# Optimization experiments

Measured on AMD Instinct MI355X. Metric: run time of the kernel, lower is better.

Reference implementation:

```python
import jax, jax.numpy as jnp
import numpy as np

N = 100000
E = 1600000
IN_DIM = 128
HID = 128
OUT = 8


def _linear_params(key, fan_in, fan_out, bias=True):
    k1, k2 = jax.random.split(key)
    bound = 1.0 / np.sqrt(fan_in)
    W = jax.random.uniform(k1, (fan_in, fan_out), jnp.float32, -bound, bound)
    if bias:
        b = jax.random.uniform(k2, (fan_out,), jnp.float32, -bound, bound)
        return W, b
    return W


def setup_inputs() -> dict:
    key = jax.random.key(0)
    ks = jax.random.split(key, 20)
    x = jax.random.normal(ks[0], (N, IN_DIM), jnp.float32)
    edge_index = jax.random.randint(ks[1], (2, E), 0, N, jnp.int64)
    y = jax.random.randint(ks[2], (N,), 0, 2, jnp.int64)
    pmp_mask = jax.random.randint(ks[3], (N,), 0, 2, jnp.int64).astype(jnp.bool_)
    # layer 1 params
    W_fr1 = _linear_params(ks[4], IN_DIM, HID, bias=False)
    W_be1 = _linear_params(ks[5], IN_DIM, HID, bias=False)
    alpha_w1, alpha_b1 = _linear_params(ks[6], IN_DIM, 1)
    Wself_w1, Wself_b1 = _linear_params(ks[7], IN_DIM, HID)
    # layer 2 params
    W_fr2 = _linear_params(ks[8], HID, HID, bias=False)
    W_be2 = _linear_params(ks[9], HID, HID, bias=False)
    alpha_w2, alpha_b2 = _linear_params(ks[10], HID, 1)
    Wself_w2, Wself_b2 = _linear_params(ks[11], HID, HID)
    # classifier
    cls_w, cls_b = _linear_params(ks[12], HID, OUT)
    return dict(x=x, edge_index=edge_index, y=y, pmp_mask=pmp_mask,
                W_fr1=W_fr1, W_be1=W_be1, alpha_w1=alpha_w1, alpha_b1=alpha_b1,
                Wself_w1=Wself_w1, Wself_b1=Wself_b1,
                W_fr2=W_fr2, W_be2=W_be2, alpha_w2=alpha_w2, alpha_b2=alpha_b2,
                Wself_w2=Wself_w2, Wself_b2=Wself_b2,
                cls_w=cls_w, cls_b=cls_b)


def _pmp_layer(x, src, dst, node_type, W_fr, W_be, alpha_w, alpha_b, Wself_w, Wself_b):
    # alpha_mlp: Linear(in,1) -> sigmoid, per node
    alpha = jax.nn.sigmoid(x @ alpha_w + alpha_b)          # [N,1]
    xj = x[src]                                            # gather source feats [E,d]
    msg_fr = xj @ W_fr                                     # [E,h]
    msg_be = xj @ W_be                                     # [E,h]
    a = alpha[dst]                                         # gather target alpha [E,1]
    ntj = node_type[src][:, None]                          # [E,1]
    msg_un = a * msg_fr + (1.0 - a) * msg_be
    msg = jnp.where(ntj == 1, msg_fr, jnp.where(ntj == 0, msg_be, msg_un))
    aggr = jax.ops.segment_sum(msg, dst, num_segments=N)   # scatter-add into targets
    return aggr + x @ Wself_w + Wself_b


def reference(x, edge_index, y, pmp_mask,
              W_fr1, W_be1, alpha_w1, alpha_b1, Wself_w1, Wself_b1,
              W_fr2, W_be2, alpha_w2, alpha_b2, Wself_w2, Wself_b2,
              cls_w, cls_b):
    src, dst = edge_index[0], edge_index[1]  # PyG: row=source j, col=target i
    node_type = jnp.where(pmp_mask, y, jnp.full_like(y, 2))  # [N], in {0,1,2}
    h = _pmp_layer(x, src, dst, node_type, W_fr1, W_be1, alpha_w1, alpha_b1, Wself_w1, Wself_b1)
    h = jax.nn.relu(h)
    # dropout inactive (inference)
    h = _pmp_layer(h, src, dst, node_type, W_fr2, W_be2, alpha_w2, alpha_b2, Wself_w2, Wself_b2)
    h = jax.nn.relu(h)
    return h @ cls_w + cls_b
```

## Files before the change

### kernel.cpp

```cpp
#include <hip/hip_runtime.h>
#include <hip/hip_bf16.h>
#include <cmath>

#define DEV static __device__ __forceinline__

constexpr int NN = 100000;
constexpr int NN_PAD = 100352;
constexpr int NE = 1600000;
constexpr int D  = 128;
constexpr int KTOT = 384;
constexpr int SCHUNK = 1024;
constexpr int NBS = (NN + SCHUNK - 1) / SCHUNK;

typedef __attribute__((ext_vector_type(8))) short short8;
typedef __attribute__((ext_vector_type(4))) float f32x4;

DEV float bf2f(unsigned short u) {
    unsigned int t = ((unsigned int)u) << 16;
    return __builtin_bit_cast(float, t);
}
DEV unsigned short f2bf(float f) {
    unsigned int u = __builtin_bit_cast(unsigned int, f);
    u += 0x7fffu + ((u >> 16) & 1u);
    return (unsigned short)(u >> 16);
}
DEV unsigned int packbf(float a, float b) {
    return (unsigned int)f2bf(a) | ((unsigned int)f2bf(b) << 16);
}

__global__ void k_detect(const unsigned int* __restrict__ ew,
                         const unsigned int* __restrict__ yw,
                         const unsigned int* __restrict__ mw,
                         int* __restrict__ flags) {
    int lane = threadIdx.x & 63;
    int c_e = __popcll(__ballot(ew[2 * lane + 1] != 0u));
    int c_y = __popcll(__ballot(yw[2 * lane + 1] != 0u));
    int c_mb = __popcll(__ballot(mw[lane] > 1u));
    int c_mz = __popcll(__ballot(mw[2 * lane + 1] != 0u));
    if (lane == 0) {
        flags[1] = (c_e < 8) ? 1 : 0;
        flags[2] = (c_y < 8) ? 1 : 0;
        flags[3] = c_mb > 8 ? 2 : (c_mz < 8 ? 1 : 0);
    }
}

__global__ void k_prep(const int* __restrict__ flg, const void* __restrict__ y,
                       const void* __restrict__ mask, int* __restrict__ nt) {
    int i = blockIdx.x * blockDim.x + threadIdx.x;
    if (i >= NN) return;
    int yv = flg[2] ? (int)((const long long*)y)[i] : ((const int*)y)[i];
    int mm = flg[3] == 2 ? (int)((const unsigned char*)mask)[i]
           : flg[3] == 1 ? (int)((const long long*)mask)[i]
           : ((const int*)mask)[i];
    nt[i] = mm ? yv : 2;
}

__global__ void k_conv_e(const int* __restrict__ flg, const void* __restrict__ ei,
                         const int* __restrict__ nt,
                         int* __restrict__ SP, int* __restrict__ DST,
                         int* __restrict__ deg, int* __restrict__ rnk) {
    int e = blockIdx.x * blockDim.x + threadIdx.x;
    if (e >= NE) return;
    int s, d;
    if (flg[1]) {
        const long long* p = (const long long*)ei;
        s = (int)p[e]; d = (int)p[NE + e];
    } else {
        const int* p = (const int*)ei;
        s = p[e]; d = p[NE + e];
    }
    SP[e] = (s << 2) | nt[s];
    DST[e] = d;
    rnk[e] = atomicAdd(&deg[d], 1);
}

__global__ void k_convx(const float* __restrict__ x,
                        unsigned short* __restrict__ Ahi, unsigned short* __restrict__ XLO) {
    long t = blockIdx.x * (long)blockDim.x + threadIdx.x;
    long g = t * 4;
    if (g >= (long)NN * D) return;
    int n = (int)(g >> 7);
    int k = (int)(g & 127);
    float4 v = *(const float4*)(x + g);
    float vv[4] = {v.x, v.y, v.z, v.w};
    ushort4 hi, lo;
    unsigned short* hp = (unsigned short*)&hi;
    unsigned short* lp = (unsigned short*)&lo;
#pragma unroll
    for (int j = 0; j < 4; j++) {
        unsigned short h = f2bf(vv[j]);
        hp[j] = h;
        lp[j] = f2bf(vv[j] - bf2f(h));
    }
    *(ushort4*)(Ahi + (size_t)n * KTOT + k) = hi;
    *(ushort4*)(XLO + (size_t)n * D + k) = lo;
}

__global__ void k_wprep(const float* __restrict__ Wsf, const float* __restrict__ Wfr,
                        const float* __restrict__ Wbe,
                        unsigned short* __restrict__ WpHi, unsigned short* __restrict__ WpLo) {
    int t = blockIdx.x * blockDim.x + threadIdx.x;
    if (t >= KTOT * D) return;
    int k = t >> 7;
    int c = t & 127;
    float w = k < 128 ? Wsf[k * 128 + c]
            : k < 256 ? Wfr[(k - 128) * 128 + c]
            : Wbe[(k - 256) * 128 + c];
    unsigned short hi = f2bf(w);
    unsigned short lo = f2bf(w - bf2f(hi));
    int kt = k >> 5, kin = k & 31;
    int grp = kin >> 3, j = kin & 7;
    int ct = c >> 4, cl = c & 15;
    size_t idx = (((size_t)kt * 8 + ct) * 64 + ((grp << 4) | cl)) * 8 + j;
    WpHi[idx] = hi;
    WpLo[idx] = lo;
}

__global__ void k_scan_a(const int* __restrict__ deg, int* __restrict__ bsum) {
    __shared__ int sh[256];
    int b = blockIdx.x, t = threadIdx.x;
    int base = b * SCHUNK + t * 4;
    int s = 0;
#pragma unroll
    for (int j = 0; j < 4; j++) { int i = base + j; if (i < NN) s += deg[i]; }
    sh[t] = s; __syncthreads();
    for (int d = 128; d > 0; d >>= 1) {
        if (t < d) sh[t] += sh[t + d];
        __syncthreads();
    }
    if (t == 0) bsum[b] = sh[0];
}

__global__ void k_scan_b(const int* __restrict__ bsum, int* __restrict__ bpre,
                         int* __restrict__ offs) {
    __shared__ int sh[128];
    int t = threadIdx.x;
    int v = (t < NBS) ? bsum[t] : 0;
    int incl = v; sh[t] = incl; __syncthreads();
    for (int d = 1; d < 128; d <<= 1) {
        int add = (t >= d) ? sh[t - d] : 0;
        __syncthreads();
        incl += add; sh[t] = incl;
        __syncthreads();
    }
    if (t < NBS) bpre[t] = incl - v;
    if (t == 0) offs[NN] = NE;
}

__global__ void k_scan_c(const int* __restrict__ deg, const int* __restrict__ bpre,
                         int* __restrict__ offs) {
    __shared__ int sh[256];
    int b = blockIdx.x, t = threadIdx.x;
    int base = b * SCHUNK + t * 4;
    int v[4];
#pragma unroll
    for (int j = 0; j < 4; j++) { int i = base + j; v[j] = (i < NN) ? deg[i] : 0; }
    int tsum = v[0] + v[1] + v[2] + v[3];
    int incl = tsum; sh[t] = incl; __syncthreads();
    for (int d = 1; d < 256; d <<= 1) {
        int add = (t >= d) ? sh[t - d] : 0;
        __syncthreads();
        incl += add; sh[t] = incl;
        __syncthreads();
    }
    int ex = (incl - tsum) + bpre[b];
#pragma unroll
    for (int j = 0; j < 4; j++) {
        int i = base + j;
        if (i < NN) { offs[i] = ex; ex += v[j]; }
    }
}

__global__ void k_place(const int* __restrict__ SP, const int* __restrict__ DST,
                        const int* __restrict__ RNK, const int* __restrict__ offs,
                        int* __restrict__ ssrc) {
    for (int e = blockIdx.x * blockDim.x + threadIdx.x; e < NE; e += gridDim.x * blockDim.x) {
        int d = DST[e];
        int slot = offs[d] + RNK[e];
        __builtin_nontemporal_store(SP[e], &ssrc[slot]);
    }
}

__global__ void __launch_bounds__(256)
k_aggr(unsigned short* __restrict__ Ahi, const unsigned short* __restrict__ XLO,
       const int* __restrict__ sp, const int* __restrict__ offs,
       const float* __restrict__ aw, const float* __restrict__ ab) {
    int lane = threadIdx.x & 63;
    int d = blockIdx.x * (blockDim.x >> 6) + (threadIdx.x >> 6);
    if (d >= NN) return;
    int eg = lane >> 4;
    int dg = lane & 15;
    int k0 = dg * 8;

    int ak = lane * 2;
    unsigned int whi = *(const unsigned int*)(Ahi + (size_t)d * KTOT + ak);
    unsigned int wlo = *(const unsigned int*)(XLO + (size_t)d * D + ak);
    float xa = bf2f((unsigned short)(whi & 0xffffu)) + bf2f((unsigned short)(wlo & 0xffffu));
    float xb = bf2f((unsigned short)(whi >> 16)) + bf2f((unsigned short)(wlo >> 16));
    float dot = xa * aw[ak] + xb * aw[ak + 1];
#pragma unroll
    for (int m = 32; m > 0; m >>= 1) dot += __shfl_xor(dot, m, 64);
    float a = 1.0f / (1.0f + expf(-(dot + ab[0])));
    float oma = 1.0f - a;

    float u[8], v[8];
#pragma unroll
    for (int q = 0; q < 8; q++) { u[q] = 0.f; v[q] = 0.f; }

    int e0 = offs[d];
    int n = offs[d + 1] - e0;
    const int* spp = sp + e0;
    for (int base = 0; base < n; base += 8) {
        int iA = base + eg;
        int iB = base + 4 + eg;
        int cA = iA < n ? iA : 0;
        int cB = iB < n ? iB : 0;
        int pkA = spp[cA];
        int pkB = spp[cB];
        int bA = pkA & 3, sA = pkA >> 2;
        int bB = pkB & 3, sB = pkB >> 2;
        float cuA = iA < n ? ((bA == 1) ? 1.f : (bA == 0 ? 0.f : a)) : 0.f;
        float cvA = iA < n ? ((bA == 0) ? 1.f : (bA == 1 ? 0.f : oma)) : 0.f;
        float cuB = iB < n ? ((bB == 1) ? 1.f : (bB == 0 ? 0.f : a)) : 0.f;
        float cvB = iB < n ? ((bB == 0) ? 1.f : (bB == 1 ? 0.f : oma)) : 0.f;
        uint4 wA = *(const uint4*)(Ahi + (size_t)sA * KTOT + k0);
        uint4 wB = *(const uint4*)(Ahi + (size_t)sB * KTOT + k0);
        const unsigned int* wa = (const unsigned int*)&wA;
        const unsigned int* wb = (const unsigned int*)&wB;
#pragma unroll
        for (int q = 0; q < 4; q++) {
            float a0 = bf2f((unsigned short)(wa[q] & 0xffffu));
            float a1 = bf2f((unsigned short)(wa[q] >> 16));
            float b0 = bf2f((unsigned short)(wb[q] & 0xffffu));
            float b1 = bf2f((unsigned short)(wb[q] >> 16));
            u[2 * q]     += cuA * a0 + cuB * b0;
            u[2 * q + 1] += cuA * a1 + cuB * b1;
            v[2 * q]     += cvA * a0 + cvB * b0;
            v[2 * q + 1] += cvA * a1 + cvB * b1;
        }
    }

#pragma unroll
    for (int q = 0; q < 8; q++) {
        u[q] += __shfl_xor(u[q], 16, 64);
        u[q] += __shfl_xor(u[q], 32, 64);
        v[q] += __shfl_xor(v[q], 16, 64);
        v[q] += __shfl_xor(v[q], 32, 64);
    }
    if (eg == 0) {
        unsigned int up[4], vp[4];
#pragma unroll
        for (int q = 0; q < 4; q++) {
            up[q] = packbf(u[2 * q], u[2 * q + 1]);
            vp[q] = packbf(v[2 * q], v[2 * q + 1]);
        }
        *(uint4*)(Ahi + (size_t)d * KTOT + 128 + k0) = *(uint4*)up;
        *(uint4*)(Ahi + (size_t)d * KTOT + 256 + k0) = *(uint4*)vp;
    }
}

__global__ void __launch_bounds__(256)
k_mfma(unsigned short* __restrict__ Ahi, unsigned short* __restrict__ XLO,
       const unsigned short* __restrict__ WpHi, const unsigned short* __restrict__ WpLo,
       const float* __restrict__ bias) {
    int lane = threadIdx.x & 63;
    int wave = threadIdx.x >> 6;
    int r0 = blockIdx.x * 256 + wave * 64;

    int mrow = lane & 15, kgrp = lane >> 4;
    const unsigned short* aHiB = Ahi + (size_t)(r0 + mrow) * KTOT + kgrp * 8;
    const unsigned short* aLoB = XLO + (size_t)(r0 + mrow) * D + kgrp * 8;

    f32x4 acc[4][8];
#pragma unroll
    for (int m = 0; m < 4; m++)
#pragma unroll
        for (int i = 0; i < 8; i++) acc[m][i] = (f32x4){0.f, 0.f, 0.f, 0.f};

#pragma unroll
    for (int kt = 0; kt < 12; kt++) {
        short8 ah[4], al[4];
#pragma unroll
        for (int m = 0; m < 4; m++) {
            ah[m] = *(const short8*)(aHiB + (size_t)m * 16 * KTOT + kt * 32);
            if (kt < 4) al[m] = *(const short8*)(aLoB + (size_t)m * 16 * D + kt * 32);
        }
#pragma unroll
        for (int ct = 0; ct < 8; ct++) {
            size_t wb = (((size_t)kt * 8 + ct) * 64 + lane) * 8;
            short8 bh = *(const short8*)(WpHi + wb);
            short8 bl = *(const short8*)(WpLo + wb);
#pragma unroll
            for (int m = 0; m < 4; m++) {
                acc[m][ct] = __builtin_amdgcn_mfma_f32_16x16x32_bf16(ah[m], bh, acc[m][ct], 0, 0, 0);
                acc[m][ct] = __builtin_amdgcn_mfma_f32_16x16x32_bf16(ah[m], bl, acc[m][ct], 0, 0, 0);
                if (kt < 4)
                    acc[m][ct] = __builtin_amdgcn_mfma_f32_16x16x32_bf16(al[m], bh, acc[m][ct], 0, 0, 0);
            }
        }
    }

    int ccol = lane & 15;
#pragma unroll
    for (int m = 0; m < 4; m++) {
        int crow = r0 + m * 16 + (lane >> 4) * 4;
#pragma unroll
        for (int ct = 0; ct < 8; ct++) {
            float bb = bias[ct * 16 + ccol];
#pragma unroll
            for (int r = 0; r < 4; r++) {
                float v = fmaxf(acc[m][ct][r] + bb, 0.f);
                unsigned short h = f2bf(v);
                unsigned short l = f2bf(v - bf2f(h));
                Ahi[(size_t)(crow + r) * KTOT + ct * 16 + ccol] = h;
                XLO[(size_t)(crow + r) * D + ct * 16 + ccol] = l;
            }
        }
    }
}

__global__ void __launch_bounds__(256)
k_cls(const unsigned short* __restrict__ Ahi, const unsigned short* __restrict__ XLO,
      const float* __restrict__ W, const float* __restrict__ b, float* __restrict__ out) {
    int lane = threadIdx.x & 63;
    int wid = blockIdx.x * (blockDim.x >> 6) + (threadIdx.x >> 6);
    if (wid >= NN) return;
    int cc = lane & 7;
    int kg = lane >> 3;
    const unsigned short* hH = Ahi + (size_t)wid * KTOT + kg * 16;
    const unsigned short* hL = XLO + (size_t)wid * D + kg * 16;
    float s = 0.f;
#pragma unroll
    for (int j = 0; j < 16; j += 2) {
        unsigned int ph = *(const unsigned int*)(hH + j);
        unsigned int pl = *(const unsigned int*)(hL + j);
        float h0 = bf2f((unsigned short)(ph & 0xffffu)) + bf2f((unsigned short)(pl & 0xffffu));
        float h1 = bf2f((unsigned short)(ph >> 16)) + bf2f((unsigned short)(pl >> 16));
        s += h0 * W[(kg * 16 + j) * 8 + cc];
        s += h1 * W[(kg * 16 + j + 1) * 8 + cc];
    }
    s += __shfl_xor(s, 8, 64);
    s += __shfl_xor(s, 16, 64);
    s += __shfl_xor(s, 32, 64);
    if (lane < 8) out[(size_t)wid * 8 + cc] = s + b[cc];
}

extern "C" void kernel_launch(void* const* d_in, const int* in_sizes, int n_in,
                              void* d_out, int out_size, void* d_ws, size_t ws_size,
                              hipStream_t stream) {
    const float* x   = (const float*)d_in[0];
    const void* ei   = d_in[1];
    const void* y    = d_in[2];
    const void* mask = d_in[3];

    char* ws = (char*)d_ws;
    size_t cur_off = 0;
    auto alloc = [&](size_t bytes) {
        size_t o = cur_off;
        cur_off = (cur_off + bytes + 255) & ~(size_t)255;
        return o;
    };

    size_t oAhi = alloc((size_t)NN_PAD * KTOT * 2);
    size_t oXLO = alloc((size_t)NN_PAD * D * 2);
    size_t oW1h = alloc(KTOT * D * 2);
    size_t oW1l = alloc(KTOT * D * 2);
    size_t oW2h = alloc(KTOT * D * 2);
    size_t oW2l = alloc(KTOT * D * 2);
    size_t oNT   = alloc(NN * 4);
    size_t oDEG  = alloc(NN * 4);
    size_t oOFFS = alloc((NN + 1) * 4);
    size_t oBSUM = alloc(NBS * 4);
    size_t oBPRE = alloc(NBS * 4);
    size_t oSP   = alloc((size_t)NE * 4);
    size_t oDST  = alloc((size_t)NE * 4);
    size_t oRNK  = alloc((size_t)NE * 4);
    size_t oSSRC = alloc((size_t)NE * 4);
    size_t oFLG  = alloc(256);

    unsigned short* Ahi = (unsigned short*)(ws + oAhi);
    unsigned short* XLO = (unsigned short*)(ws + oXLO);
    unsigned short* W1h = (unsigned short*)(ws + oW1h);
    unsigned short* W1l = (unsigned short*)(ws + oW1l);
    unsigned short* W2h = (unsigned short*)(ws + oW2h);
    unsigned short* W2l = (unsigned short*)(ws + oW2l);
    int* NT   = (int*)(ws + oNT);
    int* DEG  = (int*)(ws + oDEG);
    int* OFFS = (int*)(ws + oOFFS);
    int* BSUM = (int*)(ws + oBSUM);
    int* BPRE = (int*)(ws + oBPRE);
    int* SP   = (int*)(ws + oSP);
    int* DST  = (int*)(ws + oDST);
    int* RNK  = (int*)(ws + oRNK);
    int* SSRC = (int*)(ws + oSSRC);
    int* FLG  = (int*)(ws + oFLG);

    hipMemsetAsync(DEG, 0, NN * sizeof(int), stream);

    k_detect<<<1, 64, 0, stream>>>((const unsigned int*)ei, (const unsigned int*)y,
                                   (const unsigned int*)mask, FLG);
    k_prep<<<(NN + 255) / 256, 256, 0, stream>>>(FLG, y, mask, NT);
    k_conv_e<<<(NE + 255) / 256, 256, 0, stream>>>(FLG, ei, NT, SP, DST, DEG, RNK);
    k_convx<<<NN * D / 4 / 256, 256, 0, stream>>>(x, Ahi, XLO);
    k_wprep<<<(KTOT * D + 255) / 256, 256, 0, stream>>>(
        (const float*)d_in[8], (const float*)d_in[4], (const float*)d_in[5], W1h, W1l);
    k_wprep<<<(KTOT * D + 255) / 256, 256, 0, stream>>>(
        (const float*)d_in[14], (const float*)d_in[10], (const float*)d_in[11], W2h, W2l);

    k_scan_a<<<NBS, 256, 0, stream>>>(DEG, BSUM);
    k_scan_b<<<1, 128, 0, stream>>>(BSUM, BPRE, OFFS);
    k_scan_c<<<NBS, 256, 0, stream>>>(DEG, BPRE, OFFS);
    k_place<<<2048, 256, 0, stream>>>(SP, DST, RNK, OFFS, SSRC);

    k_aggr<<<NN / 4, 256, 0, stream>>>(Ahi, XLO, SSRC, OFFS,
        (const float*)d_in[6], (const float*)d_in[7]);
    k_mfma<<<NN_PAD / 256, 256, 0, stream>>>(Ahi, XLO, W1h, W1l, (const float*)d_in[9]);
    k_aggr<<<NN / 4, 256, 0, stream>>>(Ahi, XLO, SSRC, OFFS,
        (const float*)d_in[12], (const float*)d_in[13]);
    k_mfma<<<NN_PAD / 256, 256, 0, stream>>>(Ahi, XLO, W2h, W2l, (const float*)d_in[15]);

    k_cls<<<NN / 4, 256, 0, stream>>>(Ahi, XLO, (const float*)d_in[16],
                                      (const float*)d_in[17], (float*)d_out);
}
```

Before: 496.6 us.

## Use packed FMA in aggregation and halve rows per MFMA wave

The aggregation kernel now accumulates the alpha-weighted sum and the plain total with v_pk_fma_f32 on float pairs, and derives the (1-alpha) part as total minus alpha part. This replaces separate u/v coefficient logic and scalar FMAs. The MFMA kernel drops from 64 to 32 rows per wave and launches twice as many blocks, lowering register pressure and raising occupancy at the cost of reloading the weight tiles more often. Index arithmetic also moves from size_t to int to shorten address math.

```diff
diff --git a/kernel.cpp b/kernel.cpp
--- a/kernel.cpp
+++ b/kernel.cpp
@@ -14,6 +14,7 @@
 
 typedef __attribute__((ext_vector_type(8))) short short8;
 typedef __attribute__((ext_vector_type(4))) float f32x4;
+typedef __attribute__((ext_vector_type(2))) float f32x2;
 
 DEV float bf2f(unsigned short u) {
     unsigned int t = ((unsigned int)u) << 16;
@@ -26,6 +27,11 @@
 }
 DEV unsigned int packbf(float a, float b) {
     return (unsigned int)f2bf(a) | ((unsigned int)f2bf(b) << 16);
+}
+DEV f32x2 pk_fma(f32x2 a, f32x2 b, f32x2 c) {
+    f32x2 d;
+    asm("v_pk_fma_f32 %0, %1, %2, %3" : "=v"(d) : "v"(a), "v"(b), "v"(c));
+    return d;
 }
 
 __global__ void k_detect(const unsigned int* __restrict__ ew,
@@ -193,69 +199,73 @@
     int k0 = dg * 8;
 
     int ak = lane * 2;
-    unsigned int whi = *(const unsigned int*)(Ahi + (size_t)d * KTOT + ak);
-    unsigned int wlo = *(const unsigned int*)(XLO + (size_t)d * D + ak);
+    unsigned int whi = *(const unsigned int*)(Ahi + d * KTOT + ak);
+    unsigned int wlo = *(const unsigned int*)(XLO + d * D + ak);
     float xa = bf2f((unsigned short)(whi & 0xffffu)) + bf2f((unsigned short)(wlo & 0xffffu));
     float xb = bf2f((unsigned short)(whi >> 16)) + bf2f((unsigned short)(wlo >> 16));
     float dot = xa * aw[ak] + xb * aw[ak + 1];
 #pragma unroll
     for (int m = 32; m > 0; m >>= 1) dot += __shfl_xor(dot, m, 64);
     float a = 1.0f / (1.0f + expf(-(dot + ab[0])));
-    float oma = 1.0f - a;
-
-    float u[8], v[8];
-#pragma unroll
-    for (int q = 0; q < 8; q++) { u[q] = 0.f; v[q] = 0.f; }
+
+    f32x2 u2[4], t2[4];
+#pragma unroll
+    for (int q = 0; q < 4; q++) { u2[q] = (f32x2){0.f, 0.f}; t2[q] = (f32x2){0.f, 0.f}; }
 
     int e0 = offs[d];
     int n = offs[d + 1] - e0;
     const int* spp = sp + e0;
     for (int base = 0; base < n; base += 8) {
         int iA = base + eg;
-        int iB = base + 4 + eg;
-        int cA = iA < n ? iA : 0;
-        int cB = iB < n ? iB : 0;
-        int pkA = spp[cA];
-        int pkB = spp[cB];
+        int iB = iA + 4;
+        int pkA = spp[iA < n ? iA : 0];
+        int pkB = spp[iB < n ? iB : 0];
         int bA = pkA & 3, sA = pkA >> 2;
         int bB = pkB & 3, sB = pkB >> 2;
-        float cuA = iA < n ? ((bA == 1) ? 1.f : (bA == 0 ? 0.f : a)) : 0.f;
-        float cvA = iA < n ? ((bA == 0) ? 1.f : (bA == 1 ? 0.f : oma)) : 0.f;
-        float cuB = iB < n ? ((bB == 1) ? 1.f : (bB == 0 ? 0.f : a)) : 0.f;
-        float cvB = iB < n ? ((bB == 0) ? 1.f : (bB == 1 ? 0.f : oma)) : 0.f;
-        uint4 wA = *(const uint4*)(Ahi + (size_t)sA * KTOT + k0);
-        uint4 wB = *(const uint4*)(Ahi + (size_t)sB * KTOT + k0);
+        bool vA = iA < n, vB = iB < n;
+        float cuA = vA ? (bA == 1 ? 1.f : (bA == 2 ? a : 0.f)) : 0.f;
+        float cuB = vB ? (bB == 1 ? 1.f : (bB == 2 ? a : 0.f)) : 0.f;
+        float ctA = vA ? 1.f : 0.f;
+        float ctB = vB ? 1.f : 0.f;
+        f32x2 cuA2 = (f32x2){cuA, cuA}, cuB2 = (f32x2){cuB, cuB};
+        f32x2 ctA2 = (f32x2){ctA, ctA}, ctB2 = (f32x2){ctB, ctB};
+        uint4 wA = *(const uint4*)(Ahi + (sA * KTOT + k0));
+        uint4 wB = *(const uint4*)(Ahi + (sB * KTOT + k0));
         const unsigned int* wa = (const unsigned int*)&wA;
         const unsigned int* wb = (const unsigned int*)&wB;
 #pragma unroll
         for (int q = 0; q < 4; q++) {
-            float a0 = bf2f((unsigned short)(wa[q] & 0xffffu));
-            float a1 = bf2f((unsigned short)(wa[q] >> 16));
-            float b0 = bf2f((unsigned short)(wb[q] & 0xffffu));
-            float b1 = bf2f((unsigned short)(wb[q] >> 16));
-            u[2 * q]     += cuA * a0 + cuB * b0;
-            u[2 * q + 1] += cuA * a1 + cuB * b1;
-            v[2 * q]     += cvA * a0 + cvB * b0;
-            v[2 * q + 1] += cvA * a1 + cvB * b1;
+            f32x2 xA = (f32x2){bf2f((unsigned short)(wa[q] & 0xffffu)),
+                               bf2f((unsigned short)(wa[q] >> 16))};
+            f32x2 xB = (f32x2){bf2f((unsigned short)(wb[q] & 0xffffu)),
+                               bf2f((unsigned short)(wb[q] >> 16))};
+            u2[q] = pk_fma(xA, cuA2, u2[q]);
+            u2[q] = pk_fma(xB, cuB2, u2[q]);
+            t2[q] = pk_fma(xA, ctA2, t2[q]);
+            t2[q] = pk_fma(xB, ctB2, t2[q]);
         }
     }
 
 #pragma unroll
-    for (int q = 0; q < 8; q++) {
-        u[q] += __shfl_xor(u[q], 16, 64);
-        u[q] += __shfl_xor(u[q], 32, 64);
-        v[q] += __shfl_xor(v[q], 16, 64);
-        v[q] += __shfl_xor(v[q], 32, 64);
+    for (int q = 0; q < 4; q++) {
+        u2[q].x += __shfl_xor(u2[q].x, 16, 64);
+        u2[q].x += __shfl_xor(u2[q].x, 32, 64);
+        u2[q].y += __shfl_xor(u2[q].y, 16, 64);
+        u2[q].y += __shfl_xor(u2[q].y, 32, 64);
+        t2[q].x += __shfl_xor(t2[q].x, 16, 64);
+        t2[q].x += __shfl_xor(t2[q].x, 32, 64);
+        t2[q].y += __shfl_xor(t2[q].y, 16, 64);
+        t2[q].y += __shfl_xor(t2[q].y, 32, 64);
     }
     if (eg == 0) {
         unsigned int up[4], vp[4];
 #pragma unroll
         for (int q = 0; q < 4; q++) {
-            up[q] = packbf(u[2 * q], u[2 * q + 1]);
-            vp[q] = packbf(v[2 * q], v[2 * q + 1]);
+            up[q] = packbf(u2[q].x, u2[q].y);
+            vp[q] = packbf(t2[q].x - u2[q].x, t2[q].y - u2[q].y);
         }
-        *(uint4*)(Ahi + (size_t)d * KTOT + 128 + k0) = *(uint4*)up;
-        *(uint4*)(Ahi + (size_t)d * KTOT + 256 + k0) = *(uint4*)vp;
+        *(uint4*)(Ahi + (d * KTOT + 128 + k0)) = *(uint4*)up;
+        *(uint4*)(Ahi + (d * KTOT + 256 + k0)) = *(uint4*)vp;
     }
 }
 
@@ -265,33 +275,33 @@
        const float* __restrict__ bias) {
     int lane = threadIdx.x & 63;
     int wave = threadIdx.x >> 6;
-    int r0 = blockIdx.x * 256 + wave * 64;
+    int r0 = blockIdx.x * 128 + wave * 32;
 
     int mrow = lane & 15, kgrp = lane >> 4;
     const unsigned short* aHiB = Ahi + (size_t)(r0 + mrow) * KTOT + kgrp * 8;
     const unsigned short* aLoB = XLO + (size_t)(r0 + mrow) * D + kgrp * 8;
 
-    f32x4 acc[4][8];
-#pragma unroll
-    for (int m = 0; m < 4; m++)
+    f32x4 acc[2][8];
+#pragma unroll
+    for (int m = 0; m < 2; m++)
 #pragma unroll
         for (int i = 0; i < 8; i++) acc[m][i] = (f32x4){0.f, 0.f, 0.f, 0.f};
 
 #pragma unroll
     for (int kt = 0; kt < 12; kt++) {
-        short8 ah[4], al[4];
-#pragma unroll
-        for (int m = 0; m < 4; m++) {
+        short8 ah[2], al[2];
+#pragma unroll
+        for (int m = 0; m < 2; m++) {
             ah[m] = *(const short8*)(aHiB + (size_t)m * 16 * KTOT + kt * 32);
             if (kt < 4) al[m] = *(const short8*)(aLoB + (size_t)m * 16 * D + kt * 32);
         }
 #pragma unroll
         for (int ct = 0; ct < 8; ct++) {
-            size_t wb = (((size_t)kt * 8 + ct) * 64 + lane) * 8;
+            int wb = ((kt * 8 + ct) * 64 + lane) * 8;
             short8 bh = *(const short8*)(WpHi + wb);
             short8 bl = *(const short8*)(WpLo + wb);
 #pragma unroll
-            for (int m = 0; m < 4; m++) {
+            for (int m = 0; m < 2; m++) {
                 acc[m][ct] = __builtin_amdgcn_mfma_f32_16x16x32_bf16(ah[m], bh, acc[m][ct], 0, 0, 0);
                 acc[m][ct] = __builtin_amdgcn_mfma_f32_16x16x32_bf16(ah[m], bl, acc[m][ct], 0, 0, 0);
                 if (kt < 4)
@@ -302,7 +312,7 @@
 
     int ccol = lane & 15;
 #pragma unroll
-    for (int m = 0; m < 4; m++) {
+    for (int m = 0; m < 2; m++) {
         int crow = r0 + m * 16 + (lane >> 4) * 4;
 #pragma unroll
         for (int ct = 0; ct < 8; ct++) {
@@ -414,10 +424,10 @@
 
     k_aggr<<<NN / 4, 256, 0, stream>>>(Ahi, XLO, SSRC, OFFS,
         (const float*)d_in[6], (const float*)d_in[7]);
-    k_mfma<<<NN_PAD / 256, 256, 0, stream>>>(Ahi, XLO, W1h, W1l, (const float*)d_in[9]);
+    k_mfma<<<NN_PAD / 128, 256, 0, stream>>>(Ahi, XLO, W1h, W1l, (const float*)d_in[9]);
     k_aggr<<<NN / 4, 256, 0, stream>>>(Ahi, XLO, SSRC, OFFS,
         (const float*)d_in[12], (const float*)d_in[13]);
-    k_mfma<<<NN_PAD / 256, 256, 0, stream>>>(Ahi, XLO, W2h, W2l, (const float*)d_in[15]);
+    k_mfma<<<NN_PAD / 128, 256, 0, stream>>>(Ahi, XLO, W2h, W2l, (const float*)d_in[15]);
 
     k_cls<<<NN / 4, 256, 0, stream>>>(Ahi, XLO, (const float*)d_in[16],
                                       (const float*)d_in[17], (float*)d_out);
```

New measurement: 488.6 us. Within noise of the previous version (-1.6%).
